# Kernel optimization log

Hardware: AMD Instinct MI355X
Metric: run time of the kernel (lower is better)

The kernel has to match this reference:

```python
import jax, jax.numpy as jnp
import numpy as np

N_HEAD = 12
EPS_NORM = 1e-12   # F.normalize eps
EPS_DENOM = 1e-6   # clamp(min=1e-6)


def _l2norm(t):
    n = jnp.sqrt(jnp.sum(t * t, axis=-1, keepdims=True))
    return t / jnp.maximum(n, EPS_NORM)


def setup_inputs() -> dict:
    key = jax.random.key(0)
    ks = jax.random.split(key, 5)
    B, T, C = 1, 4096, 768
    x = jax.random.normal(ks[0], (B, T, C), dtype=jnp.float32)
    w_attn = jax.random.normal(ks[1], (C, 3 * C), dtype=jnp.float32) * 0.02
    b_attn = jnp.zeros((3 * C,), dtype=jnp.float32)
    w_proj = jax.random.normal(ks[2], (C, C), dtype=jnp.float32) * 0.02
    b_proj = jnp.zeros((C,), dtype=jnp.float32)
    return {"x": x, "w_attn": w_attn, "b_attn": b_attn,
            "w_proj": w_proj, "b_proj": b_proj}


def reference(x, w_attn, b_attn, w_proj, b_proj):
    B, T, C = x.shape
    H = N_HEAD
    hd = C // H
    qkv = x @ w_attn + b_attn                      # [B,T,3C]
    q, k, v = jnp.split(qkv, 3, axis=-1)
    # [B,T,C] -> [B,H,T,hd]
    def to_heads(t):
        return t.reshape(B, T, H, hd).transpose(0, 2, 1, 3)
    q, k, v = to_heads(q), to_heads(k), to_heads(v)
    # T > 512 branch: normalized-qk cumulative linear attention
    q = _l2norm(q)
    k = _l2norm(k)
    num = jnp.einsum('bhqd,bhkd->bhqk', q, k)      # [B,H,T,T]
    denom = jnp.maximum(jnp.cumsum(num, axis=-1), EPS_DENOM)
    att = num / denom
    y = jnp.einsum('bhqk,bhkd->bhqd', att, v)      # [B,H,T,hd]
    y = y.transpose(0, 2, 1, 3).reshape(B, T, C)
    return y @ w_proj + b_proj
```

## Files before the change

### kernel.cpp

```cpp
#include <hip/hip_runtime.h>

#define T_SEQ 4096
#define H_NUM 12
#define HD    64
#define C_DIM 768
#define N_QKV 2304
#define HT    (T_SEQ * HD)

typedef float    f32x4 __attribute__((ext_vector_type(4)));
typedef _Float16 half8 __attribute__((ext_vector_type(8)));
typedef _Float16 half4 __attribute__((ext_vector_type(4)));

#define GLDS(gp, lp) __builtin_amdgcn_global_load_lds( \
    (const __attribute__((address_space(1))) void*)(gp), \
    (__attribute__((address_space(3))) void*)(lp), 16, 0, 0)

__global__ __launch_bounds__(256) void split_x_kernel(
    const float* __restrict__ x, _Float16* __restrict__ xh,
    _Float16* __restrict__ xl, int n4)
{
    const int i = blockIdx.x * 256 + threadIdx.x;
    if (i >= n4) return;
    const float4 v = ((const float4*)x)[i];
    const float vv[4] = {v.x, v.y, v.z, v.w};
    half4 h, l;
    #pragma unroll
    for (int j = 0; j < 4; ++j) {
        const _Float16 hh = (_Float16)vv[j];
        h[j] = hh;
        l[j] = (_Float16)(vv[j] - (float)hh);
    }
    ((half4*)xh)[i] = h;
    ((half4*)xl)[i] = l;
}

__global__ __launch_bounds__(256) void split_wt_kernel(
    const float* __restrict__ W, _Float16* __restrict__ wth,
    _Float16* __restrict__ wtl)
{
    __shared__ float Ws[64][65];
    const int tid = threadIdx.x;
    const int n0 = blockIdx.x * 64, k0 = blockIdx.y * 64;
    const int lr = tid >> 4, lc = (tid & 15) << 2;
    #pragma unroll
    for (int i = 0; i < 4; ++i) {
        const float4 v = *(const float4*)(W + (size_t)(k0 + lr + i * 16) * N_QKV + n0 + lc);
        Ws[lr + i * 16][lc + 0] = v.x; Ws[lr + i * 16][lc + 1] = v.y;
        Ws[lr + i * 16][lc + 2] = v.z; Ws[lr + i * 16][lc + 3] = v.w;
    }
    __syncthreads();
    const int n = tid >> 2, ks = (tid & 3) << 4;
    half8 h0, h1, l0, l1;
    #pragma unroll
    for (int j = 0; j < 8; ++j) {
        const float v = Ws[ks + j][n];
        const _Float16 hh = (_Float16)v;
        h0[j] = hh; l0[j] = (_Float16)(v - (float)hh);
    }
    #pragma unroll
    for (int j = 0; j < 8; ++j) {
        const float v = Ws[ks + 8 + j][n];
        const _Float16 hh = (_Float16)v;
        h1[j] = hh; l1[j] = (_Float16)(v - (float)hh);
    }
    const size_t dst = (size_t)(n0 + n) * C_DIM + k0 + ks;
    *(half8*)(wth + dst) = h0; *(half8*)(wth + dst + 8) = h1;
    *(half8*)(wtl + dst) = l0; *(half8*)(wtl + dst + 8) = l1;
}

__global__ __launch_bounds__(256) void gemm_qkv_kernel(
    const _Float16* __restrict__ xh, const _Float16* __restrict__ xl,
    const _Float16* __restrict__ wth, const _Float16* __restrict__ wtl,
    const float* __restrict__ bias,
    _Float16* __restrict__ qhi, _Float16* __restrict__ qlo,
    _Float16* __restrict__ khi, _Float16* __restrict__ klo,
    _Float16* __restrict__ vt)
{
    __shared__ __align__(16) _Float16 AH[128 * 64];
    __shared__ __align__(16) _Float16 AL[128 * 64];
    __shared__ __align__(16) _Float16 BH[64 * 64];
    __shared__ __align__(16) _Float16 BL[64 * 64];
    const int tid = threadIdx.x;
    const int wv = tid >> 6, lane = tid & 63;
    const int fm = lane & 15, fg = lane >> 4;
    const int lrow = lane >> 3;
    const int lcs  = (lane & 7) ^ (lrow & 7);
    const int bx = blockIdx.x;
    const int m0 = blockIdx.y * 128;

    auto dma_chunk = [&](int c) {
        const int kc0 = c * 64;
        #pragma unroll
        for (int i = 0; i < 12; ++i) {
            const int qidx = wv * 12 + i;
            if (qidx < 16) {
                const int rg = qidx;
                GLDS(xh + (size_t)(m0 + rg * 8 + lrow) * C_DIM + kc0 + lcs * 8, &AH[rg * 512]);
            } else if (qidx < 32) {
                const int rg = qidx - 16;
                GLDS(xl + (size_t)(m0 + rg * 8 + lrow) * C_DIM + kc0 + lcs * 8, &AL[rg * 512]);
            } else if (qidx < 40) {
                const int rg = qidx - 32;
                GLDS(wth + (size_t)(bx * 64 + rg * 8 + lrow) * C_DIM + kc0 + lcs * 8, &BH[rg * 512]);
            } else {
                const int rg = qidx - 40;
                GLDS(wtl + (size_t)(bx * 64 + rg * 8 + lrow) * C_DIM + kc0 + lcs * 8, &BL[rg * 512]);
            }
        }
    };

    f32x4 acc[2][4];
    #pragma unroll
    for (int mt = 0; mt < 2; ++mt)
        #pragma unroll
        for (int ct = 0; ct < 4; ++ct) acc[mt][ct] = (f32x4){0.f, 0.f, 0.f, 0.f};

    const int swz = fm & 7;
    dma_chunk(0);
    #pragma unroll 1
    for (int c = 0; c < C_DIM / 64; ++c) {
        __syncthreads();
        half8 ah[2][2], al[2][2], bh[4][2], bl[4][2];
        #pragma unroll
        for (int mt = 0; mt < 2; ++mt) {
            const int rb = (wv * 32 + mt * 16 + fm) * 64;
            #pragma unroll
            for (int kc = 0; kc < 2; ++kc) {
                const int cb = ((kc * 4 + fg) ^ swz) * 8;
                ah[mt][kc] = *(const half8*)&AH[rb + cb];
                al[mt][kc] = *(const half8*)&AL[rb + cb];
            }
        }
        #pragma unroll
        for (int ct = 0; ct < 4; ++ct) {
            const int rb = (ct * 16 + fm) * 64;
            #pragma unroll
            for (int kc = 0; kc < 2; ++kc) {
                const int cb = ((kc * 4 + fg) ^ swz) * 8;
                bh[ct][kc] = *(const half8*)&BH[rb + cb];
                bl[ct][kc] = *(const half8*)&BL[rb + cb];
            }
        }
        __syncthreads();
        if (c + 1 < C_DIM / 64) dma_chunk(c + 1);
        #pragma unroll
        for (int mt = 0; mt < 2; ++mt)
            #pragma unroll
            for (int ct = 0; ct < 4; ++ct)
                #pragma unroll
                for (int kc = 0; kc < 2; ++kc) {
                    acc[mt][ct] = __builtin_amdgcn_mfma_f32_16x16x32_f16(ah[mt][kc], bh[ct][kc], acc[mt][ct], 0, 0, 0);
                    acc[mt][ct] = __builtin_amdgcn_mfma_f32_16x16x32_f16(ah[mt][kc], bl[ct][kc], acc[mt][ct], 0, 0, 0);
                    acc[mt][ct] = __builtin_amdgcn_mfma_f32_16x16x32_f16(al[mt][kc], bh[ct][kc], acc[mt][ct], 0, 0, 0);
                }
    }

    const int sec = bx / 12, h = bx % 12;
    const size_t hb = (size_t)h * HT;
    float bb[4];
    #pragma unroll
    for (int ct = 0; ct < 4; ++ct) bb[ct] = bias[bx * 64 + ct * 16 + fm];

    if (sec < 2) {
        _Float16* dh = (sec == 0) ? qhi : khi;
        _Float16* dl = (sec == 0) ? qlo : klo;
        #pragma unroll
        for (int mt = 0; mt < 2; ++mt)
            #pragma unroll
            for (int r = 0; r < 4; ++r) {
                float o[4];
                float ss = 0.f;
                #pragma unroll
                for (int ct = 0; ct < 4; ++ct) {
                    o[ct] = acc[mt][ct][r] + bb[ct];
                    ss += o[ct] * o[ct];
                }
                #pragma unroll
                for (int mk = 1; mk < 16; mk <<= 1) ss += __shfl_xor(ss, mk, 16);
                const float invn = 1.0f / fmaxf(sqrtf(ss), 1e-12f);
                const int t = m0 + wv * 32 + mt * 16 + fg * 4 + r;
                const size_t rb = hb + (size_t)t * HD;
                #pragma unroll
                for (int ct = 0; ct < 4; ++ct) {
                    const float v = o[ct] * invn;
                    const _Float16 vh = (_Float16)v;
                    dh[rb + ct * 16 + fm] = vh;
                    dl[rb + ct * 16 + fm] = (_Float16)(v - (float)vh);
                }
            }
    } else {
        #pragma unroll
        for (int mt = 0; mt < 2; ++mt) {
            const int t0 = m0 + wv * 32 + mt * 16 + fg * 4;
            #pragma unroll
            for (int ct = 0; ct < 4; ++ct) {
                half4 pk;
                #pragma unroll
                for (int r = 0; r < 4; ++r) pk[r] = (_Float16)(acc[mt][ct][r] + bb[ct]);
                *(half4*)(vt + hb + (size_t)(ct * 16 + fm) * T_SEQ + t0) = pk;
            }
        }
    }
}

__global__ __launch_bounds__(256) void attn_kernel(
    const _Float16* __restrict__ qhi, const _Float16* __restrict__ qlo,
    const _Float16* __restrict__ khi, const _Float16* __restrict__ klo,
    const _Float16* __restrict__ vt,  _Float16* __restrict__ ylin)
{
    __shared__ __align__(16) _Float16 KH[64 * 64];
    __shared__ __align__(16) _Float16 KL[64 * 64];
    __shared__ __align__(16) _Float16 VS[64 * 64];
    __shared__ __align__(16) _Float16 P2[64][72];

    const int tid = threadIdx.x;
    const int wv = tid >> 6, lane = tid & 63;
    const int fm = lane & 15, fg = lane >> 4;
    const int lrow = lane >> 3;
    const int lcs  = (lane & 7) ^ (lrow & 7);
    const int h = blockIdx.y, qt = blockIdx.x;
    const size_t hb = (size_t)h * HT;

    const int q = qt * 64 + wv * 16 + fm;
    half8 qf[2][2];
    #pragma unroll
    for (int kc = 0; kc < 2; ++kc) {
        const size_t off = hb + (size_t)q * HD + kc * 32 + fg * 8;
        qf[0][kc] = *(const half8*)(qhi + off);
        qf[1][kc] = *(const half8*)(qlo + off);
    }

    auto dma_tile = [&](int kt) {
        const size_t kb = hb + (size_t)kt * 64 * HD;
        const int vcol = kt * 64;
        #pragma unroll
        for (int i = 0; i < 6; ++i) {
            const int qidx = wv * 6 + i;
            const int rg = qidx & 7;
            if (qidx < 8) {
                GLDS(khi + kb + (size_t)(rg * 8 + lrow) * HD + lcs * 8, &KH[rg * 512]);
            } else if (qidx < 16) {
                GLDS(klo + kb + (size_t)(rg * 8 + lrow) * HD + lcs * 8, &KL[rg * 512]);
            } else {
                GLDS(vt + hb + (size_t)(rg * 8 + lrow) * T_SEQ + vcol + lcs * 8, &VS[rg * 512]);
            }
        }
    };

    f32x4 yacc[4];
    #pragma unroll
    for (int ct = 0; ct < 4; ++ct) yacc[ct] = (f32x4){0.f, 0.f, 0.f, 0.f};
    float carry = 0.0f;
    const int swz = fm & 7;

    dma_tile(0);
    #pragma unroll 1
    for (int kt = 0; kt < T_SEQ / 64; ++kt) {
        __syncthreads();
        half8 ka[4][2], kl[4][2], vf[4][2];
        #pragma unroll
        for (int kr = 0; kr < 4; ++kr) {
            const int rb = (kr * 16 + fm) * 64;
            #pragma unroll
            for (int kc = 0; kc < 2; ++kc) {
                const int cb = ((kc * 4 + fg) ^ swz) * 8;
                ka[kr][kc] = *(const half8*)&KH[rb + cb];
                kl[kr][kc] = *(const half8*)&KL[rb + cb];
            }
        }
        #pragma unroll
        for (int ct = 0; ct < 4; ++ct) {
            const int rb = (ct * 16 + fm) * 64;
            #pragma unroll
            for (int kc = 0; kc < 2; ++kc)
                vf[ct][kc] = *(const half8*)&VS[rb + (((kc * 4 + fg) ^ swz) * 8)];
        }
        __syncthreads();
        if (kt + 1 < T_SEQ / 64) dma_tile(kt + 1);

        f32x4 sacc[4];
        #pragma unroll
        for (int kr = 0; kr < 4; ++kr) sacc[kr] = (f32x4){0.f, 0.f, 0.f, 0.f};
        #pragma unroll
        for (int kr = 0; kr < 4; ++kr)
            #pragma unroll
            for (int kc = 0; kc < 2; ++kc) {
                sacc[kr] = __builtin_amdgcn_mfma_f32_16x16x32_f16(ka[kr][kc], qf[0][kc], sacc[kr], 0, 0, 0);
                sacc[kr] = __builtin_amdgcn_mfma_f32_16x16x32_f16(ka[kr][kc], qf[1][kc], sacc[kr], 0, 0, 0);
                sacc[kr] = __builtin_amdgcn_mfma_f32_16x16x32_f16(kl[kr][kc], qf[0][kc], sacc[kr], 0, 0, 0);
            }

        #pragma unroll
        for (int kr = 0; kr < 4; ++kr) {
            const float s0 = sacc[kr][0], s1 = sacc[kr][1];
            const float s2 = sacc[kr][2], s3 = sacc[kr][3];
            const float p1 = s0 + s1, p2 = p1 + s2, p3 = p2 + s3;
            const float u1 = __shfl_xor(p3, 16, 64);
            const float pair = p3 + u1;
            const float u2 = __shfl_xor(pair, 32, 64);
            const float tot16 = pair + u2;
            const float pref = ((fg & 1) ? u1 : 0.0f) + ((fg & 2) ? u2 : 0.0f);
            const float base = carry + pref;
            carry += tot16;
            const float a0 = s0 * __builtin_amdgcn_rcpf(fmaxf(base + s0, 1e-6f));
            const float a1 = s1 * __builtin_amdgcn_rcpf(fmaxf(base + p1, 1e-6f));
            const float a2 = s2 * __builtin_amdgcn_rcpf(fmaxf(base + p2, 1e-6f));
            const float a3 = s3 * __builtin_amdgcn_rcpf(fmaxf(base + p3, 1e-6f));
            half4 pk = {(_Float16)(a0 * 0.03125f), (_Float16)(a1 * 0.03125f),
                        (_Float16)(a2 * 0.03125f), (_Float16)(a3 * 0.03125f)};
            *(half4*)&P2[wv * 16 + fm][kr * 16 + fg * 4] = pk;
        }

        #pragma unroll
        for (int kc = 0; kc < 2; ++kc) {
            const half8 af = *(const half8*)&P2[wv * 16 + fm][kc * 32 + fg * 8];
            #pragma unroll
            for (int ct = 0; ct < 4; ++ct)
                yacc[ct] = __builtin_amdgcn_mfma_f32_16x16x32_f16(af, vf[ct][kc], yacc[ct], 0, 0, 0);
        }
    }

    #pragma unroll
    for (int ct = 0; ct < 4; ++ct)
        #pragma unroll
        for (int r = 0; r < 4; ++r) {
            const int t = qt * 64 + wv * 16 + fg * 4 + r;
            ylin[(size_t)t * C_DIM + h * HD + ct * 16 + fm] =
                (_Float16)(yacc[ct][r] * 0.0078125f);
        }
}

__global__ __launch_bounds__(256) void gemm_proj_kernel(
    const _Float16* __restrict__ A, const float* __restrict__ W,
    const float* __restrict__ bias, float* __restrict__ out)
{
    __shared__ _Float16 As[64][72];
    __shared__ _Float16 Bt[64][72];
    typedef _Float16 half2v __attribute__((ext_vector_type(2)));
    const int tid = threadIdx.x;
    const int w = tid >> 6, lane = tid & 63;
    const int m = lane & 15, g = lane >> 4;
    const int row0 = blockIdx.x << 6, col0 = blockIdx.y << 6;
    const int ar = tid >> 3, ac8 = (tid & 7) << 3;
    const int bn0 = (tid & 15) << 2, bpv = tid >> 4;
    f32x4 acc[4];
    #pragma unroll
    for (int ct = 0; ct < 4; ++ct) acc[ct] = (f32x4){0.f, 0.f, 0.f, 0.f};

    for (int kt = 0; kt < C_DIM; kt += 64) {
        half8 av0 = *(const half8*)(A + (size_t)(row0 + ar)      * C_DIM + kt + ac8);
        half8 av1 = *(const half8*)(A + (size_t)(row0 + ar + 32) * C_DIM + kt + ac8);
        float4 w0[2], w1[2];
        #pragma unroll
        for (int i = 0; i < 2; ++i) {
            const int k = kt + 2 * (bpv + 16 * i);
            w0[i] = *(const float4*)(W + (size_t)k       * C_DIM + col0 + bn0);
            w1[i] = *(const float4*)(W + (size_t)(k + 1) * C_DIM + col0 + bn0);
        }
        __syncthreads();
        *(half8*)&As[ar][ac8]      = av0;
        *(half8*)&As[ar + 32][ac8] = av1;
        #pragma unroll
        for (int i = 0; i < 2; ++i) {
            const int p = bpv + 16 * i;
            const float a_[4] = {w0[i].x, w0[i].y, w0[i].z, w0[i].w};
            const float b_[4] = {w1[i].x, w1[i].y, w1[i].z, w1[i].w};
            #pragma unroll
            for (int u = 0; u < 4; ++u) {
                half2v pk = {(_Float16)a_[u], (_Float16)b_[u]};
                *(half2v*)&Bt[bn0 + u][2 * p] = pk;
            }
        }
        __syncthreads();
        #pragma unroll
        for (int kc = 0; kc < 2; ++kc) {
            const half8 a = *(half8*)&As[w * 16 + m][kc * 32 + g * 8];
            #pragma unroll
            for (int ct = 0; ct < 4; ++ct) {
                const half8 b = *(half8*)&Bt[ct * 16 + m][kc * 32 + g * 8];
                acc[ct] = __builtin_amdgcn_mfma_f32_16x16x32_f16(a, b, acc[ct], 0, 0, 0);
            }
        }
    }
    #pragma unroll
    for (int ct = 0; ct < 4; ++ct)
        #pragma unroll
        for (int r = 0; r < 4; ++r) {
            const int t = row0 + w * 16 + g * 4 + r;
            const int n = col0 + ct * 16 + m;
            out[(size_t)t * C_DIM + n] = acc[ct][r] * 4096.0f + bias[n];
        }
}

extern "C" void kernel_launch(void* const* d_in, const int* in_sizes, int n_in,
                              void* d_out, int out_size, void* d_ws, size_t ws_size,
                              hipStream_t stream)
{
    const float* x      = (const float*)d_in[0];
    const float* w_attn = (const float*)d_in[1];
    const float* b_attn = (const float*)d_in[2];
    const float* w_proj = (const float*)d_in[3];
    const float* b_proj = (const float*)d_in[4];
    float* out = (float*)d_out;

    const size_t perQK = (size_t)H_NUM * HT;
    const size_t perX  = (size_t)T_SEQ * C_DIM;
    const size_t perW  = (size_t)N_QKV * C_DIM;
    _Float16* base = (_Float16*)d_ws;
    _Float16* xhi  = base;
    _Float16* xlo  = xhi + perX;
    _Float16* wthi = xlo + perX;
    _Float16* wtlo = wthi + perW;
    _Float16* qhi  = wtlo + perW;
    _Float16* qlo  = qhi + perQK;
    _Float16* khi  = qlo + perQK;
    _Float16* klo  = khi + perQK;
    _Float16* vtp  = klo + perQK;
    _Float16* ylin = xhi;

    split_x_kernel<<<(perX / 4 + 255) / 256, 256, 0, stream>>>(x, xhi, xlo, perX / 4);
    split_wt_kernel<<<dim3(N_QKV / 64, C_DIM / 64), 256, 0, stream>>>(w_attn, wthi, wtlo);
    gemm_qkv_kernel<<<dim3(N_QKV / 64, T_SEQ / 128), 256, 0, stream>>>(
        xhi, xlo, wthi, wtlo, b_attn, qhi, qlo, khi, klo, vtp);
    attn_kernel<<<dim3(T_SEQ / 64, H_NUM), 256, 0, stream>>>(
        qhi, qlo, khi, klo, vtp, ylin);
    gemm_proj_kernel<<<dim3(T_SEQ / 64, C_DIM / 64), 256, 0, stream>>>(
        ylin, w_proj, b_proj, out);
}
```

Measured before the change: 324.2 us.

## Split attention key range in two using precomputed key-sum prefix carry

New measurement: 1.084 ms. 234% more time.

```diff
diff --git a/kernel.cpp b/kernel.cpp
--- a/kernel.cpp
+++ b/kernel.cpp
@@ -6,14 +6,26 @@
 #define C_DIM 768
 #define N_QKV 2304
 #define HT    (T_SEQ * HD)
+#define NSPLIT 2
+#define KT_PER (T_SEQ / 64 / NSPLIT)
 
 typedef float    f32x4 __attribute__((ext_vector_type(4)));
 typedef _Float16 half8 __attribute__((ext_vector_type(8)));
 typedef _Float16 half4 __attribute__((ext_vector_type(4)));
+typedef _Float16 half2v __attribute__((ext_vector_type(2)));
+typedef __fp16   fp16x2 __attribute__((ext_vector_type(2)));
+typedef unsigned uint4v __attribute__((ext_vector_type(4)));
 
 #define GLDS(gp, lp) __builtin_amdgcn_global_load_lds( \
     (const __attribute__((address_space(1))) void*)(gp), \
     (__attribute__((address_space(3))) void*)(lp), 16, 0, 0)
+
+__device__ __forceinline__ void permlane32_swap(unsigned& a, unsigned& b) {
+    asm("v_permlane32_swap_b32 %0, %1" : "+v"(a), "+v"(b));
+}
+__device__ __forceinline__ void permlane16_swap(unsigned& a, unsigned& b) {
+    asm("v_permlane16_swap_b32 %0, %1" : "+v"(a), "+v"(b));
+}
 
 __global__ __launch_bounds__(256) void split_x_kernel(
     const float* __restrict__ x, _Float16* __restrict__ xh,
@@ -203,22 +215,52 @@
     }
 }
 
-__global__ __launch_bounds__(256) void attn_kernel(
+__global__ __launch_bounds__(256) void ksum_kernel(
+    const _Float16* __restrict__ khi, const _Float16* __restrict__ klo,
+    float* __restrict__ kpref)
+{
+    __shared__ float red[32][64];
+    const int h = blockIdx.x;
+    const int tid = threadIdx.x;
+    const int r0 = tid >> 3;
+    const int c0 = (tid & 7) * 8;
+    const size_t hb = (size_t)h * HT;
+    float acc[8] = {0.f, 0.f, 0.f, 0.f, 0.f, 0.f, 0.f, 0.f};
+    #pragma unroll 4
+    for (int it = 0; it < (KT_PER * 64) / 32; ++it) {
+        const size_t off = hb + (size_t)(it * 32 + r0) * HD + c0;
+        const half8 a = *(const half8*)(khi + off);
+        const half8 b = *(const half8*)(klo + off);
+        #pragma unroll
+        for (int j = 0; j < 8; ++j) acc[j] += (float)a[j] + (float)b[j];
+    }
+    #pragma unroll
+    for (int j = 0; j < 8; ++j) red[r0][c0 + j] = acc[j];
+    __syncthreads();
+    if (tid < 64) {
+        float s = 0.f;
+        #pragma unroll
+        for (int r = 0; r < 32; ++r) s += red[r][tid];
+        kpref[h * HD + tid] = s;
+    }
+}
+
+__global__ __launch_bounds__(256, 5) void attn_kernel(
     const _Float16* __restrict__ qhi, const _Float16* __restrict__ qlo,
     const _Float16* __restrict__ khi, const _Float16* __restrict__ klo,
-    const _Float16* __restrict__ vt,  _Float16* __restrict__ ylin)
+    const _Float16* __restrict__ vt,  const float* __restrict__ kpref,
+    _Float16* __restrict__ yp0, _Float16* __restrict__ yp1)
 {
     __shared__ __align__(16) _Float16 KH[64 * 64];
     __shared__ __align__(16) _Float16 KL[64 * 64];
     __shared__ __align__(16) _Float16 VS[64 * 64];
-    __shared__ __align__(16) _Float16 P2[64][72];
 
     const int tid = threadIdx.x;
     const int wv = tid >> 6, lane = tid & 63;
     const int fm = lane & 15, fg = lane >> 4;
     const int lrow = lane >> 3;
     const int lcs  = (lane & 7) ^ (lrow & 7);
-    const int h = blockIdx.y, qt = blockIdx.x;
+    const int h = blockIdx.y, qt = blockIdx.x, z = blockIdx.z;
     const size_t hb = (size_t)h * HT;
 
     const int q = qt * 64 + wv * 16 + fm;
@@ -228,6 +270,25 @@
         const size_t off = hb + (size_t)q * HD + kc * 32 + fg * 8;
         qf[0][kc] = *(const half8*)(qhi + off);
         qf[1][kc] = *(const half8*)(qlo + off);
+    }
+
+    float carry = 0.0f;
+    if (z) {
+        const float* kp = kpref + h * HD + fg * 16;
+        const size_t qoff = hb + (size_t)q * HD + fg * 16;
+        const half8 qh0 = *(const half8*)(qhi + qoff);
+        const half8 qh1 = *(const half8*)(qhi + qoff + 8);
+        const half8 ql0 = *(const half8*)(qlo + qoff);
+        const half8 ql1 = *(const half8*)(qlo + qoff + 8);
+        float s = 0.f;
+        #pragma unroll
+        for (int j = 0; j < 8; ++j) {
+            s += ((float)qh0[j] + (float)ql0[j]) * kp[j];
+            s += ((float)qh1[j] + (float)ql1[j]) * kp[8 + j];
+        }
+        s += __shfl_xor(s, 16, 64);
+        s += __shfl_xor(s, 32, 64);
+        carry = s;
     }
 
     auto dma_tile = [&](int kt) {
@@ -250,12 +311,13 @@
     f32x4 yacc[4];
     #pragma unroll
     for (int ct = 0; ct < 4; ++ct) yacc[ct] = (f32x4){0.f, 0.f, 0.f, 0.f};
-    float carry = 0.0f;
     const int swz = fm & 7;
-
-    dma_tile(0);
+    const int kt0 = z * KT_PER;
+
+    dma_tile(kt0);
     #pragma unroll 1
-    for (int kt = 0; kt < T_SEQ / 64; ++kt) {
+    for (int kk = 0; kk < KT_PER; ++kk) {
+        const int kt = kt0 + kk;
         __syncthreads();
         half8 ka[4][2], kl[4][2], vf[4][2];
         #pragma unroll
@@ -276,7 +338,7 @@
                 vf[ct][kc] = *(const half8*)&VS[rb + (((kc * 4 + fg) ^ swz) * 8)];
         }
         __syncthreads();
-        if (kt + 1 < T_SEQ / 64) dma_tile(kt + 1);
+        if (kk + 1 < KT_PER) dma_tile(kt + 1);
 
         f32x4 sacc[4];
         #pragma unroll
@@ -290,6 +352,7 @@
                 sacc[kr] = __builtin_amdgcn_mfma_f32_16x16x32_f16(kl[kr][kc], qf[0][kc], sacc[kr], 0, 0, 0);
             }
 
+        unsigned pk[4][2];
         #pragma unroll
         for (int kr = 0; kr < 4; ++kr) {
             const float s0 = sacc[kr][0], s1 = sacc[kr][1];
@@ -306,37 +369,49 @@
             const float a1 = s1 * __builtin_amdgcn_rcpf(fmaxf(base + p1, 1e-6f));
             const float a2 = s2 * __builtin_amdgcn_rcpf(fmaxf(base + p2, 1e-6f));
             const float a3 = s3 * __builtin_amdgcn_rcpf(fmaxf(base + p3, 1e-6f));
-            half4 pk = {(_Float16)(a0 * 0.03125f), (_Float16)(a1 * 0.03125f),
-                        (_Float16)(a2 * 0.03125f), (_Float16)(a3 * 0.03125f)};
-            *(half4*)&P2[wv * 16 + fm][kr * 16 + fg * 4] = pk;
-        }
+            const fp16x2 c0 = __builtin_amdgcn_cvt_pkrtz(a0 * 0.03125f, a1 * 0.03125f);
+            const fp16x2 c1 = __builtin_amdgcn_cvt_pkrtz(a2 * 0.03125f, a3 * 0.03125f);
+            pk[kr][0] = __builtin_bit_cast(unsigned, c0);
+            pk[kr][1] = __builtin_bit_cast(unsigned, c1);
+        }
+
+        #pragma unroll
+        for (int g = 0; g < 2; ++g)
+            #pragma unroll
+            for (int hh = 0; hh < 2; ++hh) {
+                permlane32_swap(pk[g * 2 + 0][hh], pk[g * 2 + 1][hh]);
+                permlane16_swap(pk[g * 2 + 0][hh], pk[g * 2 + 1][hh]);
+            }
 
         #pragma unroll
         for (int kc = 0; kc < 2; ++kc) {
-            const half8 af = *(const half8*)&P2[wv * 16 + fm][kc * 32 + fg * 8];
+            const uint4v u = {pk[2 * kc][0], pk[2 * kc][1],
+                              pk[2 * kc + 1][0], pk[2 * kc + 1][1]};
+            const half8 af = __builtin_bit_cast(half8, u);
             #pragma unroll
             for (int ct = 0; ct < 4; ++ct)
                 yacc[ct] = __builtin_amdgcn_mfma_f32_16x16x32_f16(af, vf[ct][kc], yacc[ct], 0, 0, 0);
         }
     }
 
+    _Float16* __restrict__ yp = z ? yp1 : yp0;
     #pragma unroll
     for (int ct = 0; ct < 4; ++ct)
         #pragma unroll
         for (int r = 0; r < 4; ++r) {
             const int t = qt * 64 + wv * 16 + fg * 4 + r;
-            ylin[(size_t)t * C_DIM + h * HD + ct * 16 + fm] =
+            yp[(size_t)t * C_DIM + h * HD + ct * 16 + fm] =
                 (_Float16)(yacc[ct][r] * 0.0078125f);
         }
 }
 
 __global__ __launch_bounds__(256) void gemm_proj_kernel(
-    const _Float16* __restrict__ A, const float* __restrict__ W,
-    const float* __restrict__ bias, float* __restrict__ out)
+    const _Float16* __restrict__ A0, const _Float16* __restrict__ A1,
+    const float* __restrict__ W, const float* __restrict__ bias,
+    float* __restrict__ out)
 {
     __shared__ _Float16 As[64][72];
     __shared__ _Float16 Bt[64][72];
-    typedef _Float16 half2v __attribute__((ext_vector_type(2)));
     const int tid = threadIdx.x;
     const int w = tid >> 6, lane = tid & 63;
     const int m = lane & 15, g = lane >> 4;
@@ -348,8 +423,10 @@
     for (int ct = 0; ct < 4; ++ct) acc[ct] = (f32x4){0.f, 0.f, 0.f, 0.f};
 
     for (int kt = 0; kt < C_DIM; kt += 64) {
-        half8 av0 = *(const half8*)(A + (size_t)(row0 + ar)      * C_DIM + kt + ac8);
-        half8 av1 = *(const half8*)(A + (size_t)(row0 + ar + 32) * C_DIM + kt + ac8);
+        const size_t i0 = (size_t)(row0 + ar) * C_DIM + kt + ac8;
+        const size_t i1 = (size_t)(row0 + ar + 32) * C_DIM + kt + ac8;
+        half8 av0 = *(const half8*)(A0 + i0) + *(const half8*)(A1 + i0);
+        half8 av1 = *(const half8*)(A0 + i1) + *(const half8*)(A1 + i1);
         float4 w0[2], w1[2];
         #pragma unroll
         for (int i = 0; i < 2; ++i) {
@@ -416,14 +493,17 @@
     _Float16* khi  = qlo + perQK;
     _Float16* klo  = khi + perQK;
     _Float16* vtp  = klo + perQK;
-    _Float16* ylin = xhi;
+    float*    kpref = (float*)wthi;
+    _Float16* yp0  = xhi;
+    _Float16* yp1  = xlo;
 
     split_x_kernel<<<(perX / 4 + 255) / 256, 256, 0, stream>>>(x, xhi, xlo, perX / 4);
     split_wt_kernel<<<dim3(N_QKV / 64, C_DIM / 64), 256, 0, stream>>>(w_attn, wthi, wtlo);
     gemm_qkv_kernel<<<dim3(N_QKV / 64, T_SEQ / 128), 256, 0, stream>>>(
         xhi, xlo, wthi, wtlo, b_attn, qhi, qlo, khi, klo, vtp);
-    attn_kernel<<<dim3(T_SEQ / 64, H_NUM), 256, 0, stream>>>(
-        qhi, qlo, khi, klo, vtp, ylin);
+    ksum_kernel<<<dim3(H_NUM), 256, 0, stream>>>(khi, klo, kpref);
+    attn_kernel<<<dim3(T_SEQ / 64, H_NUM, NSPLIT), 256, 0, stream>>>(
+        qhi, qlo, khi, klo, vtp, kpref, yp0, yp1);
     gemm_proj_kernel<<<dim3(T_SEQ / 64, C_DIM / 64), 256, 0, stream>>>(
-        ylin, w_proj, b_proj, out);
-}
+        yp0, yp1, w_proj, b_proj, out);
+}
```

## Double-buffer K/V tiles and reshuffle P in registers via permlane swaps

Applied to the files above, without the earlier changes.

Result: faster. 300.6 us (-7.3%).

```diff
diff --git a/kernel.cpp b/kernel.cpp
--- a/kernel.cpp
+++ b/kernel.cpp
@@ -6,14 +6,25 @@
 #define C_DIM 768
 #define N_QKV 2304
 #define HT    (T_SEQ * HD)
+#define KT_TOT (T_SEQ / 64)
 
 typedef float    f32x4 __attribute__((ext_vector_type(4)));
 typedef _Float16 half8 __attribute__((ext_vector_type(8)));
 typedef _Float16 half4 __attribute__((ext_vector_type(4)));
+typedef _Float16 half2v __attribute__((ext_vector_type(2)));
+typedef __fp16   fp16x2 __attribute__((ext_vector_type(2)));
+typedef unsigned uint4v __attribute__((ext_vector_type(4)));
 
 #define GLDS(gp, lp) __builtin_amdgcn_global_load_lds( \
     (const __attribute__((address_space(1))) void*)(gp), \
     (__attribute__((address_space(3))) void*)(lp), 16, 0, 0)
+
+__device__ __forceinline__ void permlane32_swap(unsigned& a, unsigned& b) {
+    asm("v_permlane32_swap_b32 %0, %1" : "+v"(a), "+v"(b));
+}
+__device__ __forceinline__ void permlane16_swap(unsigned& a, unsigned& b) {
+    asm("v_permlane16_swap_b32 %0, %1" : "+v"(a), "+v"(b));
+}
 
 __global__ __launch_bounds__(256) void split_x_kernel(
     const float* __restrict__ x, _Float16* __restrict__ xh,
@@ -208,10 +219,9 @@
     const _Float16* __restrict__ khi, const _Float16* __restrict__ klo,
     const _Float16* __restrict__ vt,  _Float16* __restrict__ ylin)
 {
-    __shared__ __align__(16) _Float16 KH[64 * 64];
-    __shared__ __align__(16) _Float16 KL[64 * 64];
-    __shared__ __align__(16) _Float16 VS[64 * 64];
-    __shared__ __align__(16) _Float16 P2[64][72];
+    __shared__ __align__(16) _Float16 KH[2][64 * 64];
+    __shared__ __align__(16) _Float16 KL[2][64 * 64];
+    __shared__ __align__(16) _Float16 VS[2][64 * 64];
 
     const int tid = threadIdx.x;
     const int wv = tid >> 6, lane = tid & 63;
@@ -230,7 +240,7 @@
         qf[1][kc] = *(const half8*)(qlo + off);
     }
 
-    auto dma_tile = [&](int kt) {
+    auto dma_tile = [&](int kt, int buf) {
         const size_t kb = hb + (size_t)kt * 64 * HD;
         const int vcol = kt * 64;
         #pragma unroll
@@ -238,11 +248,11 @@
             const int qidx = wv * 6 + i;
             const int rg = qidx & 7;
             if (qidx < 8) {
-                GLDS(khi + kb + (size_t)(rg * 8 + lrow) * HD + lcs * 8, &KH[rg * 512]);
+                GLDS(khi + kb + (size_t)(rg * 8 + lrow) * HD + lcs * 8, &KH[buf][rg * 512]);
             } else if (qidx < 16) {
-                GLDS(klo + kb + (size_t)(rg * 8 + lrow) * HD + lcs * 8, &KL[rg * 512]);
+                GLDS(klo + kb + (size_t)(rg * 8 + lrow) * HD + lcs * 8, &KL[buf][rg * 512]);
             } else {
-                GLDS(vt + hb + (size_t)(rg * 8 + lrow) * T_SEQ + vcol + lcs * 8, &VS[rg * 512]);
+                GLDS(vt + hb + (size_t)(rg * 8 + lrow) * T_SEQ + vcol + lcs * 8, &VS[buf][rg * 512]);
             }
         }
     };
@@ -253,10 +263,13 @@
     float carry = 0.0f;
     const int swz = fm & 7;
 
-    dma_tile(0);
+    int cur = 0;
+    dma_tile(0, 0);
     #pragma unroll 1
-    for (int kt = 0; kt < T_SEQ / 64; ++kt) {
+    for (int kt = 0; kt < KT_TOT; ++kt) {
         __syncthreads();
+        if (kt + 1 < KT_TOT) dma_tile(kt + 1, cur ^ 1);
+
         half8 ka[4][2], kl[4][2], vf[4][2];
         #pragma unroll
         for (int kr = 0; kr < 4; ++kr) {
@@ -264,8 +277,8 @@
             #pragma unroll
             for (int kc = 0; kc < 2; ++kc) {
                 const int cb = ((kc * 4 + fg) ^ swz) * 8;
-                ka[kr][kc] = *(const half8*)&KH[rb + cb];
-                kl[kr][kc] = *(const half8*)&KL[rb + cb];
+                ka[kr][kc] = *(const half8*)&KH[cur][rb + cb];
+                kl[kr][kc] = *(const half8*)&KL[cur][rb + cb];
             }
         }
         #pragma unroll
@@ -273,10 +286,8 @@
             const int rb = (ct * 16 + fm) * 64;
             #pragma unroll
             for (int kc = 0; kc < 2; ++kc)
-                vf[ct][kc] = *(const half8*)&VS[rb + (((kc * 4 + fg) ^ swz) * 8)];
-        }
-        __syncthreads();
-        if (kt + 1 < T_SEQ / 64) dma_tile(kt + 1);
+                vf[ct][kc] = *(const half8*)&VS[cur][rb + (((kc * 4 + fg) ^ swz) * 8)];
+        }
 
         f32x4 sacc[4];
         #pragma unroll
@@ -290,6 +301,7 @@
                 sacc[kr] = __builtin_amdgcn_mfma_f32_16x16x32_f16(kl[kr][kc], qf[0][kc], sacc[kr], 0, 0, 0);
             }
 
+        unsigned pk[4][2];
         #pragma unroll
         for (int kr = 0; kr < 4; ++kr) {
             const float s0 = sacc[kr][0], s1 = sacc[kr][1];
@@ -306,18 +318,30 @@
             const float a1 = s1 * __builtin_amdgcn_rcpf(fmaxf(base + p1, 1e-6f));
             const float a2 = s2 * __builtin_amdgcn_rcpf(fmaxf(base + p2, 1e-6f));
             const float a3 = s3 * __builtin_amdgcn_rcpf(fmaxf(base + p3, 1e-6f));
-            half4 pk = {(_Float16)(a0 * 0.03125f), (_Float16)(a1 * 0.03125f),
-                        (_Float16)(a2 * 0.03125f), (_Float16)(a3 * 0.03125f)};
-            *(half4*)&P2[wv * 16 + fm][kr * 16 + fg * 4] = pk;
-        }
+            const fp16x2 c0 = __builtin_amdgcn_cvt_pkrtz(a0 * 0.03125f, a1 * 0.03125f);
+            const fp16x2 c1 = __builtin_amdgcn_cvt_pkrtz(a2 * 0.03125f, a3 * 0.03125f);
+            pk[kr][0] = __builtin_bit_cast(unsigned, c0);
+            pk[kr][1] = __builtin_bit_cast(unsigned, c1);
+        }
+
+        #pragma unroll
+        for (int g = 0; g < 2; ++g)
+            #pragma unroll
+            for (int hh = 0; hh < 2; ++hh) {
+                permlane32_swap(pk[g * 2 + 0][hh], pk[g * 2 + 1][hh]);
+                permlane16_swap(pk[g * 2 + 0][hh], pk[g * 2 + 1][hh]);
+            }
 
         #pragma unroll
         for (int kc = 0; kc < 2; ++kc) {
-            const half8 af = *(const half8*)&P2[wv * 16 + fm][kc * 32 + fg * 8];
+            const uint4v u = {pk[2 * kc][0], pk[2 * kc][1],
+                              pk[2 * kc + 1][0], pk[2 * kc + 1][1]};
+            const half8 af = __builtin_bit_cast(half8, u);
             #pragma unroll
             for (int ct = 0; ct < 4; ++ct)
                 yacc[ct] = __builtin_amdgcn_mfma_f32_16x16x32_f16(af, vf[ct][kc], yacc[ct], 0, 0, 0);
         }
+        cur ^= 1;
     }
 
     #pragma unroll
@@ -336,7 +360,6 @@
 {
     __shared__ _Float16 As[64][72];
     __shared__ _Float16 Bt[64][72];
-    typedef _Float16 half2v __attribute__((ext_vector_type(2)));
     const int tid = threadIdx.x;
     const int w = tid >> 6, lane = tid & 63;
     const int m = lane & 15, g = lane >> 4;
```
